# Performance work log

Measured on AMD Instinct MI355X. Metric: run time of the kernel, lower is better.

## Reference

```python
import jax, jax.numpy as jnp
import numpy as np

RADIUS = 1.5
PARTITION_NUM = 5
OUT_CHANNEL = 128
IN_CHANNEL = 64
EPS = 1e-5


def setup_inputs() -> dict:
    key = jax.random.key(0)
    ks = jax.random.split(key, 10)
    B, N, npoint, K = 16, 8192, 2048, 32
    D = 61  # points feature dim; in_channel = D + 3 = 64
    xyz = jax.random.normal(ks[0], (B, N, 3), dtype=jnp.float32)
    points = jax.random.normal(ks[1], (B, N, D), dtype=jnp.float32)
    local_coordinates = jax.random.uniform(ks[2], (B, npoint, K, 3), dtype=jnp.float32)
    neighbor_lists = jax.random.randint(ks[3], (B, npoint, K), 0, N)
    data_idx = jax.random.randint(ks[4], (B, npoint), 0, N)
    parameter_list = jnp.zeros((1,), dtype=jnp.float32)
    # params (torch Linear stored transposed here: [in, out])
    W1 = jax.random.normal(ks[5], (IN_CHANNEL * PARTITION_NUM, OUT_CHANNEL), dtype=jnp.float32) * 0.02
    b1 = jnp.zeros((OUT_CHANNEL,), dtype=jnp.float32)
    g1 = jnp.ones((OUT_CHANNEL,), dtype=jnp.float32)
    be1 = jnp.zeros((OUT_CHANNEL,), dtype=jnp.float32)
    W2 = jax.random.normal(ks[6], (OUT_CHANNEL, OUT_CHANNEL), dtype=jnp.float32) * 0.02
    b2 = jnp.zeros((OUT_CHANNEL,), dtype=jnp.float32)
    g2 = jnp.ones((OUT_CHANNEL,), dtype=jnp.float32)
    be2 = jnp.zeros((OUT_CHANNEL,), dtype=jnp.float32)
    return dict(xyz=xyz, points=points, local_coordinates=local_coordinates,
                neighbor_lists=neighbor_lists, parameter_list=parameter_list,
                data_idx=data_idx, W1=W1, b1=b1, g1=g1, be1=be1,
                W2=W2, b2=b2, g2=g2, be2=be2)


def _forward(xyz, points, local_coordinates, parameter_list,
             W1, b1, g1, be1, W2, b2, g2, be2, neighbor_lists, data_idx):
    B, N, _ = xyz.shape
    _, npoint, K = neighbor_lists.shape
    # new_xyz = index_points(xyz, data_idx)
    new_xyz = jnp.take_along_axis(xyz, data_idx[:, :, None], axis=1)  # [B, npoint, 3]
    # points = cat(points, xyz) -> in_channel features
    pts = jnp.concatenate([points, xyz], axis=2)  # [B, N, C]
    C = pts.shape[-1]
    # gather neighbor feats: [B, npoint, K, C] (permute chain in torch is a net identity)
    idx = neighbor_lists.reshape(B, npoint * K)
    grouped = jnp.take_along_axis(pts, idx[:, :, None], axis=1).reshape(B, npoint, K, C)
    # circle_conv: radial binning + scatter-add over partition bins
    lc = local_coordinates.reshape(B, npoint, K, 3)
    dist = jnp.linalg.norm(lc[..., 0:2], axis=-1)          # [B, npoint, K]
    dist = jnp.minimum(dist / RADIUS, 0.99)                # cut(x, 0.99)
    bins = jnp.floor(dist * PARTITION_NUM).astype(jnp.int32)
    onehot = jax.nn.one_hot(bins, PARTITION_NUM, dtype=grouped.dtype)  # [B, npoint, K, P]
    feature = jnp.einsum('bnkp,bnkc->bnpc', onehot, grouped)           # scatter_add
    feature = feature.reshape(B * npoint, PARTITION_NUM * C)
    # Linear + BatchNorm1d (training-mode batch stats) + ReLU
    x = feature @ W1 + b1                                  # [B*npoint, out]
    mu = x.mean(axis=0)
    var = x.var(axis=0)
    x = jax.nn.relu(g1 * (x - mu) / jnp.sqrt(var + EPS) + be1)
    x = x.reshape(B, npoint, -1)
    # Linear + BatchNorm1d over channels + ReLU
    y = x @ W2 + b2                                        # [B, npoint, out]
    mu2 = y.mean(axis=(0, 1))
    var2 = y.var(axis=(0, 1))
    new_points = jax.nn.relu(g2 * (y - mu2) / jnp.sqrt(var2 + EPS) + be2)
    return new_xyz, new_points


def reference(xyz, points, local_coordinates, neighbor_lists, parameter_list,
              data_idx, W1, b1, g1, be1, W2, b2, g2, be2):
    return _forward(xyz, points, local_coordinates, parameter_list,
                    W1, b1, g1, be1, W2, b2, g2, be2, neighbor_lists, data_idx)
```

## Files before the change

### kernel.cpp

```cpp
#include <hip/hip_runtime.h>
#include <hip/hip_bf16.h>
#include <math.h>

#define B_SZ     16
#define N_PTS    8192
#define NPOINT   2048
#define KNBR     32
#define D_FEAT   61
#define C_IN     64
#define P_BINS   5
#define C_OUT    128
#define M_ROWS   (B_SZ * NPOINT)
#define K1       (C_IN * P_BINS)
#define EPSV     1e-5f
#define NREP     16

typedef __attribute__((ext_vector_type(8))) short bf16x8;
typedef __attribute__((ext_vector_type(4))) float f32x4;

__device__ __forceinline__ unsigned short f2bf_rne(float v) {
    unsigned u = __float_as_uint(v);
    u += 0x7fffu + ((u >> 16) & 1u);
    return (unsigned short)(u >> 16);
}
__device__ __forceinline__ float bf2f(unsigned short v) {
    return __uint_as_float(((unsigned)v) << 16);
}

__device__ __forceinline__ size_t fragB_idx(int n, int c) {
    return ((size_t)((c >> 5) * 8 + (n >> 4)) << 9) +
           ((((c >> 3) & 3) * 16 + (n & 15)) << 3) + (c & 7);
}

__global__ __launch_bounds__(256) void prep_kernel(
    const float* __restrict__ points, const float* __restrict__ xyz,
    const float* __restrict__ W1, const float* __restrict__ W2,
    unsigned short* __restrict__ ptsb, unsigned short* __restrict__ W1f,
    unsigned short* __restrict__ W2f, float* __restrict__ st)
{
    const int blk = blockIdx.x;
    const int tid = threadIdx.x;
    if (blk < 32768) {
        const int xcd  = blk & 7;
        const int slot = blk >> 3;
        const int b    = 2 * xcd + (slot >> 11);
        const int rin  = (slot & 2047) * 4 + (tid >> 6);
        const int row  = b * N_PTS + rin;
        const int c    = tid & 63;
        float v;
        if (c < D_FEAT) v = points[(size_t)row * D_FEAT + c];
        else            v = xyz[(size_t)row * 3 + (c - D_FEAT)];
        ptsb[((size_t)row << 6) | c] = f2bf_rne(v);
    } else {
        const int gid = (blk - 32768) * 256 + tid;
        if (gid < 40960) {
            int c = gid >> 7, n = gid & 127;
            W1f[fragB_idx(n, c)] = f2bf_rne(W1[gid]);
        } else if (gid < 57344) {
            int i = gid - 40960;
            int c = i >> 7, n = i & 127;
            W2f[fragB_idx(n, c)] = f2bf_rne(W2[i]);
        } else {
            st[gid - 57344] = 0.f;
        }
    }
}

__global__ __launch_bounds__(256) void fusedg1_kernel(
    const unsigned short* __restrict__ ptsb, const float* __restrict__ xyz,
    const float* __restrict__ lc, const int* __restrict__ nl,
    const int* __restrict__ didx, const unsigned short* __restrict__ W1f,
    const float* __restrict__ b1, unsigned short* __restrict__ x1f,
    float* __restrict__ st, float* __restrict__ newxyz)
{
    const int g    = blockIdx.x;
    const int xcd  = g & 7;
    const int slot = g >> 3;
    const int b    = 2 * xcd + (slot >> 7);
    const int tile = b * 128 + (slot & 127);
    const int wave = threadIdx.x >> 6;
    const int lane = threadIdx.x & 63;
    const int k    = lane & 31;
    const int lm   = lane & 15, kg = lane >> 4;
    const int kgl  = (lane >> 3) & 3, jl = lane & 7, khalf = lane >> 5;

    __shared__ int s_srt[4][32];
    __shared__ __align__(16) unsigned short sA[10 * 512];

    const unsigned short* __restrict__ tb = ptsb + (((size_t)b * N_PTS) << 6);
    const float* __restrict__ xbase = xyz + (size_t)b * N_PTS * 3;

    for (int p = 0; p < 4; ++p) {
        const int mloc = wave * 4 + p;
        const int bid  = tile * 16 + mloc;
        const size_t nbase = (size_t)bid * KNBR;

        const float x = lc[(nbase + k) * 3 + 0];
        const float y = lc[(nbase + k) * 3 + 1];
        const float dd = fminf(sqrtf(x * x + y * y) * (1.0f / 1.5f), 0.99f);
        int bin = (int)(dd * 5.0f);
        bin = bin > 4 ? 4 : (bin < 0 ? 0 : bin);
        const int n = nl[nbase + k];

        unsigned m0 = (unsigned)__ballot(bin == 0);
        unsigned m1 = (unsigned)__ballot(bin == 1);
        unsigned m2 = (unsigned)__ballot(bin == 2);
        unsigned m3 = (unsigned)__ballot(bin == 3);
        unsigned m4 = (unsigned)__ballot(bin == 4);
        const int c0n = __popc(m0), c1n = __popc(m1);
        const int c2n = __popc(m2), c3n = __popc(m3);
        const int e0 = c0n, e1 = e0 + c1n, e2 = e1 + c2n, e3 = e2 + c3n;

        int start = (bin > 0 ? c0n : 0) + (bin > 1 ? c1n : 0) +
                    (bin > 2 ? c2n : 0) + (bin > 3 ? c3n : 0);
        unsigned mymask = m0;
        mymask = bin == 1 ? m1 : mymask;
        mymask = bin == 2 ? m2 : mymask;
        mymask = bin == 3 ? m3 : mymask;
        mymask = bin == 4 ? m4 : mymask;
        const int pos = start + __popc(mymask & ((1u << k) - 1u));

        if (lane < 32) s_srt[wave][pos] = n;
        if (lane >= 32 && lane < 35) {
            const int di = didx[bid];
            newxyz[(size_t)bid * 3 + (lane - 32)] = xbase[(size_t)di * 3 + (lane - 32)];
        }

        const int srtv = s_srt[wave][k];

        unsigned short vv[32];
        #pragma unroll
        for (int kk = 0; kk < 32; ++kk) {
            const int nr = __builtin_amdgcn_readlane(srtv, kk);
            vv[kk] = tb[((size_t)nr << 6) | lane];
        }

        float a0 = 0.f, a1 = 0.f, a2 = 0.f, a3 = 0.f, a4 = 0.f;
        #pragma unroll
        for (int kk = 0; kk < 32; ++kk) {
            const float v = bf2f(vv[kk]);
            if      (kk < e0) a0 += v;
            else if (kk < e1) a1 += v;
            else if (kk < e2) a2 += v;
            else if (kk < e3) a3 += v;
            else              a4 += v;
        }

        const float vals[5] = {a0, a1, a2, a3, a4};
        #pragma unroll
        for (int bb = 0; bb < 5; ++bb) {
            const int kb = bb * 2 + khalf;
            sA[kb * 512 + (kgl * 16 + mloc) * 8 + jl] = f2bf_rne(vals[bb]);
        }
    }
    __syncthreads();

    f32x4 acc0 = {}, acc1 = {};
    #pragma unroll
    for (int kb = 0; kb < 10; ++kb) {
        bf16x8 a = *(const bf16x8*)&sA[kb * 512 + lane * 8];
        bf16x8 w0 = *(const bf16x8*)(W1f + ((size_t)(kb * 8 + wave * 2) << 9) + lane * 8);
        bf16x8 w1 = *(const bf16x8*)(W1f + ((size_t)(kb * 8 + wave * 2 + 1) << 9) + lane * 8);
        acc0 = __builtin_amdgcn_mfma_f32_16x16x32_bf16(a, w0, acc0, 0, 0, 0);
        acc1 = __builtin_amdgcn_mfma_f32_16x16x32_bf16(a, w1, acc1, 0, 0, 0);
    }

    const int rep = (g & (NREP - 1)) * 128;
    #pragma unroll
    for (int q = 0; q < 2; ++q) {
        const f32x4 A = q ? acc1 : acc0;
        const int col = (wave * 2 + q) * 16 + lm;
        const float bb = b1[col];
        float ls = 0.f, lq = 0.f;
        #pragma unroll
        for (int i = 0; i < 4; ++i) {
            float vv2 = A[i] + bb;
            const size_t idx = (((size_t)(tile * 4 + (col >> 5))) << 9) +
                               ((((col >> 3) & 3) * 16 + kg * 4 + i) << 3) + (col & 7);
            x1f[idx] = f2bf_rne(vv2);
            ls += vv2; lq += vv2 * vv2;
        }
        ls += __shfl_xor(ls, 16); ls += __shfl_xor(ls, 32);
        lq += __shfl_xor(lq, 16); lq += __shfl_xor(lq, 32);
        if (kg == 0) {
            atomicAdd(&st[rep + col], ls);
            atomicAdd(&st[2048 + rep + col], lq);
        }
    }
}

__global__ __launch_bounds__(256) void gemm2_mfma(
    const unsigned short* __restrict__ Xf,
    const float* __restrict__ st_in,
    const float* __restrict__ g1, const float* __restrict__ be1,
    const unsigned short* __restrict__ Wf, const float* __restrict__ bias,
    unsigned short* __restrict__ out, float* __restrict__ st)
{
    __shared__ float sc[128], sh[128];
    const int tid = threadIdx.x;
    if (tid < 128) {
        float s = 0.f, q = 0.f;
        #pragma unroll
        for (int r = 0; r < NREP; ++r) {
            s += st_in[r * 128 + tid];
            q += st_in[2048 + r * 128 + tid];
        }
        float mu  = s * (1.0f / (float)M_ROWS);
        float var = q * (1.0f / (float)M_ROWS) - mu * mu;
        float iv  = 1.0f / sqrtf(var + EPSV);
        float sg  = g1[tid] * iv;
        sc[tid] = sg;
        sh[tid] = be1[tid] - mu * sg;
    }
    __syncthreads();

    const int g    = blockIdx.x;
    const int xcd  = g & 7;
    const int slot = g >> 3;
    const int b    = 2 * xcd + (slot >> 7);
    const int tile = b * 128 + (slot & 127);

    const int wave = tid >> 6, lane = tid & 63;
    const int lm = lane & 15, kg = lane >> 4;

    f32x4 acc0 = {}, acc1 = {};
    #pragma unroll
    for (int kb = 0; kb < 4; ++kb) {
        const int c0 = kb * 32 + kg * 8;
        bf16x8 xr = *(const bf16x8*)(Xf + (((size_t)(tile * 4 + kb)) << 9) + lane * 8);
        bf16x8 a;
        #pragma unroll
        for (int j = 0; j < 8; ++j) {
            float xv = bf2f((unsigned short)xr[j]);
            a[j] = (short)f2bf_rne(fmaxf(0.f, sc[c0 + j] * xv + sh[c0 + j]));
        }
        bf16x8 w0 = *(const bf16x8*)(Wf + ((size_t)(kb * 8 + wave * 2) << 9) + lane * 8);
        bf16x8 w1 = *(const bf16x8*)(Wf + ((size_t)(kb * 8 + wave * 2 + 1) << 9) + lane * 8);
        acc0 = __builtin_amdgcn_mfma_f32_16x16x32_bf16(a, w0, acc0, 0, 0, 0);
        acc1 = __builtin_amdgcn_mfma_f32_16x16x32_bf16(a, w1, acc1, 0, 0, 0);
    }

    const int orow = tile * 16 + kg * 4;
    const int rep = (g & (NREP - 1)) * 128;
    #pragma unroll
    for (int q = 0; q < 2; ++q) {
        const f32x4 A = q ? acc1 : acc0;
        const int col = (wave * 2 + q) * 16 + lm;
        const float bb = bias[col];
        float ls = 0.f, lq = 0.f;
        #pragma unroll
        for (int i = 0; i < 4; ++i) {
            float v = A[i] + bb;
            out[(size_t)(orow + i) * C_OUT + col] = f2bf_rne(v);
            ls += v; lq += v * v;
        }
        ls += __shfl_xor(ls, 16); ls += __shfl_xor(ls, 32);
        lq += __shfl_xor(lq, 16); lq += __shfl_xor(lq, 32);
        if (kg == 0) {
            atomicAdd(&st[4096 + rep + col], ls);
            atomicAdd(&st[6144 + rep + col], lq);
        }
    }
}

__global__ __launch_bounds__(256) void out_kernel(
    const unsigned short* __restrict__ Y, const float* __restrict__ st,
    const float* __restrict__ g2, const float* __restrict__ be2,
    float* __restrict__ out)
{
    __shared__ float sc[128], sh[128];
    const int tid = threadIdx.x;
    if (tid < 128) {
        float s = 0.f, q = 0.f;
        #pragma unroll
        for (int r = 0; r < NREP; ++r) {
            s += st[4096 + r * 128 + tid];
            q += st[6144 + r * 128 + tid];
        }
        float mu  = s * (1.0f / (float)M_ROWS);
        float var = q * (1.0f / (float)M_ROWS) - mu * mu;
        float iv  = 1.0f / sqrtf(var + EPSV);
        float sg  = g2[tid] * iv;
        sc[tid] = sg;
        sh[tid] = be2[tid] - mu * sg;
    }
    __syncthreads();

    const size_t e8 = (size_t)blockIdx.x * 256 + tid;
    bf16x8 v = ((const bf16x8*)Y)[e8];
    const int cb = (int)((e8 * 8) & 127);
    float4 r0, r1;
    r0.x = fmaxf(0.f, sc[cb + 0] * bf2f((unsigned short)v[0]) + sh[cb + 0]);
    r0.y = fmaxf(0.f, sc[cb + 1] * bf2f((unsigned short)v[1]) + sh[cb + 1]);
    r0.z = fmaxf(0.f, sc[cb + 2] * bf2f((unsigned short)v[2]) + sh[cb + 2]);
    r0.w = fmaxf(0.f, sc[cb + 3] * bf2f((unsigned short)v[3]) + sh[cb + 3]);
    r1.x = fmaxf(0.f, sc[cb + 4] * bf2f((unsigned short)v[4]) + sh[cb + 4]);
    r1.y = fmaxf(0.f, sc[cb + 5] * bf2f((unsigned short)v[5]) + sh[cb + 5]);
    r1.z = fmaxf(0.f, sc[cb + 6] * bf2f((unsigned short)v[6]) + sh[cb + 6]);
    r1.w = fmaxf(0.f, sc[cb + 7] * bf2f((unsigned short)v[7]) + sh[cb + 7]);
    ((float4*)out)[e8 * 2]     = r0;
    ((float4*)out)[e8 * 2 + 1] = r1;
}

extern "C" void kernel_launch(void* const* d_in, const int* in_sizes, int n_in,
                              void* d_out, int out_size, void* d_ws, size_t ws_size,
                              hipStream_t stream)
{
    const float* xyz    = (const float*)d_in[0];
    const float* points = (const float*)d_in[1];
    const float* lc     = (const float*)d_in[2];
    const int*   nl     = (const int*)d_in[3];
    const int*   didx   = (const int*)d_in[5];
    const float* W1     = (const float*)d_in[6];
    const float* b1     = (const float*)d_in[7];
    const float* g1     = (const float*)d_in[8];
    const float* be1    = (const float*)d_in[9];
    const float* W2     = (const float*)d_in[10];
    const float* b2     = (const float*)d_in[11];
    const float* g2     = (const float*)d_in[12];
    const float* be2    = (const float*)d_in[13];

    float* out = (float*)d_out;
    char*  ws  = (char*)d_ws;

    unsigned short* ptsb = (unsigned short*)ws;
    unsigned short* x1f  = (unsigned short*)(ws + 16777216);
    unsigned short* yb   = (unsigned short*)(ws + 25165824);
    unsigned short* W1f  = (unsigned short*)(ws + 33554432);
    unsigned short* W2f  = (unsigned short*)(ws + 33636352);
    float*          st   = (float*)(ws + 33669120);

    prep_kernel<<<32768 + 256, 256, 0, stream>>>(points, xyz, W1, W2,
                                                 ptsb, W1f, W2f, st);
    fusedg1_kernel<<<M_ROWS / 16, 256, 0, stream>>>(ptsb, xyz, lc, nl, didx,
                                                    W1f, b1, x1f, st, out);
    gemm2_mfma<<<M_ROWS / 16, 256, 0, stream>>>(x1f, st, g1, be1,
                                                W2f, b2, yb, st);
    out_kernel<<<(M_ROWS * C_OUT) / (256 * 8), 256, 0, stream>>>(
        yb, st, g2, be2, out + (size_t)M_ROWS * 3);
}
```

Measured before the change: 188.1 us.

## Vectorize neighbor gathers via LDS staging and retile gemm2 per-wave with block-reduced stats

Neighbor feature rows are now fetched as 16-byte vector loads, 8 lanes per row, and staged through shared memory. This replaces 32 scalar 2-byte gathers per lane. gemm2 now assigns each wave its own 16-row tile covering all 128 columns, launches 4x fewer blocks, and reduces BN statistics across waves in LDS before issuing atomics. The stat replication factor drops from 16 to 8, which cuts atomic traffic but raises contention per slot, and the extra LDS staging adds shared-memory use and a read-after-write dependency within each wave.

After: 186.6 us. No clear change (-0.8%).

```diff
diff --git a/kernel.cpp b/kernel.cpp
--- a/kernel.cpp
+++ b/kernel.cpp
@@ -13,7 +13,6 @@
 #define M_ROWS   (B_SZ * NPOINT)
 #define K1       (C_IN * P_BINS)
 #define EPSV     1e-5f
-#define NREP     16
 
 typedef __attribute__((ext_vector_type(8))) short bf16x8;
 typedef __attribute__((ext_vector_type(4))) float f32x4;
@@ -60,7 +59,7 @@
             int i = gid - 40960;
             int c = i >> 7, n = i & 127;
             W2f[fragB_idx(n, c)] = f2bf_rne(W2[i]);
-        } else {
+        } else if (gid < 61440) {
             st[gid - 57344] = 0.f;
         }
     }
@@ -85,6 +84,7 @@
     const int kgl  = (lane >> 3) & 3, jl = lane & 7, khalf = lane >> 5;
 
     __shared__ int s_srt[4][32];
+    __shared__ __align__(16) unsigned short s_stage[4][32][64];
     __shared__ __align__(16) unsigned short sA[10 * 512];
 
     const unsigned short* __restrict__ tb = ptsb + (((size_t)b * N_PTS) << 6);
@@ -126,19 +126,18 @@
             newxyz[(size_t)bid * 3 + (lane - 32)] = xbase[(size_t)di * 3 + (lane - 32)];
         }
 
-        const int srtv = s_srt[wave][k];
-
-        unsigned short vv[32];
+        const int r = lane >> 3, j7 = lane & 7;
+        #pragma unroll
+        for (int g4 = 0; g4 < 4; ++g4) {
+            const int nr = s_srt[wave][g4 * 8 + r];
+            bf16x8 row = *(const bf16x8*)(tb + ((size_t)nr << 6) + j7 * 8);
+            *(bf16x8*)&s_stage[wave][g4 * 8 + r][j7 * 8] = row;
+        }
+
+        float a0 = 0.f, a1 = 0.f, a2 = 0.f, a3 = 0.f, a4 = 0.f;
         #pragma unroll
         for (int kk = 0; kk < 32; ++kk) {
-            const int nr = __builtin_amdgcn_readlane(srtv, kk);
-            vv[kk] = tb[((size_t)nr << 6) | lane];
-        }
-
-        float a0 = 0.f, a1 = 0.f, a2 = 0.f, a3 = 0.f, a4 = 0.f;
-        #pragma unroll
-        for (int kk = 0; kk < 32; ++kk) {
-            const float v = bf2f(vv[kk]);
+            const float v = bf2f(s_stage[wave][kk][lane]);
             if      (kk < e0) a0 += v;
             else if (kk < e1) a1 += v;
             else if (kk < e2) a2 += v;
@@ -165,7 +164,7 @@
         acc1 = __builtin_amdgcn_mfma_f32_16x16x32_bf16(a, w1, acc1, 0, 0, 0);
     }
 
-    const int rep = (g & (NREP - 1)) * 128;
+    const int rep = (g & 7) * 128;
     #pragma unroll
     for (int q = 0; q < 2; ++q) {
         const f32x4 A = q ? acc1 : acc0;
@@ -184,7 +183,7 @@
         lq += __shfl_xor(lq, 16); lq += __shfl_xor(lq, 32);
         if (kg == 0) {
             atomicAdd(&st[rep + col], ls);
-            atomicAdd(&st[2048 + rep + col], lq);
+            atomicAdd(&st[1024 + rep + col], lq);
         }
     }
 }
@@ -197,13 +196,14 @@
     unsigned short* __restrict__ out, float* __restrict__ st)
 {
     __shared__ float sc[128], sh[128];
+    __shared__ float s_s[4][128], s_q[4][128];
     const int tid = threadIdx.x;
     if (tid < 128) {
         float s = 0.f, q = 0.f;
         #pragma unroll
-        for (int r = 0; r < NREP; ++r) {
+        for (int r = 0; r < 8; ++r) {
             s += st_in[r * 128 + tid];
-            q += st_in[2048 + r * 128 + tid];
+            q += st_in[1024 + r * 128 + tid];
         }
         float mu  = s * (1.0f / (float)M_ROWS);
         float var = q * (1.0f / (float)M_ROWS) - mu * mu;
@@ -217,13 +217,13 @@
     const int g    = blockIdx.x;
     const int xcd  = g & 7;
     const int slot = g >> 3;
-    const int b    = 2 * xcd + (slot >> 7);
-    const int tile = b * 128 + (slot & 127);
+    const int bb_  = 2 * xcd + (slot >> 5);
+    const int tile = (bb_ * 32 + (slot & 31)) * 4 + (tid >> 6);
 
     const int wave = tid >> 6, lane = tid & 63;
     const int lm = lane & 15, kg = lane >> 4;
 
-    f32x4 acc0 = {}, acc1 = {};
+    f32x4 acc[8] = {};
     #pragma unroll
     for (int kb = 0; kb < 4; ++kb) {
         const int c0 = kb * 32 + kg * 8;
@@ -234,32 +234,36 @@
             float xv = bf2f((unsigned short)xr[j]);
             a[j] = (short)f2bf_rne(fmaxf(0.f, sc[c0 + j] * xv + sh[c0 + j]));
         }
-        bf16x8 w0 = *(const bf16x8*)(Wf + ((size_t)(kb * 8 + wave * 2) << 9) + lane * 8);
-        bf16x8 w1 = *(const bf16x8*)(Wf + ((size_t)(kb * 8 + wave * 2 + 1) << 9) + lane * 8);
-        acc0 = __builtin_amdgcn_mfma_f32_16x16x32_bf16(a, w0, acc0, 0, 0, 0);
-        acc1 = __builtin_amdgcn_mfma_f32_16x16x32_bf16(a, w1, acc1, 0, 0, 0);
+        #pragma unroll
+        for (int nf = 0; nf < 8; ++nf) {
+            bf16x8 bfr = *(const bf16x8*)(Wf + (((size_t)(kb * 8 + nf)) << 9) + lane * 8);
+            acc[nf] = __builtin_amdgcn_mfma_f32_16x16x32_bf16(a, bfr, acc[nf], 0, 0, 0);
+        }
     }
 
     const int orow = tile * 16 + kg * 4;
-    const int rep = (g & (NREP - 1)) * 128;
     #pragma unroll
-    for (int q = 0; q < 2; ++q) {
-        const f32x4 A = q ? acc1 : acc0;
-        const int col = (wave * 2 + q) * 16 + lm;
+    for (int nf = 0; nf < 8; ++nf) {
+        const int col = nf * 16 + lm;
         const float bb = bias[col];
         float ls = 0.f, lq = 0.f;
         #pragma unroll
         for (int i = 0; i < 4; ++i) {
-            float v = A[i] + bb;
+            float v = acc[nf][i] + bb;
             out[(size_t)(orow + i) * C_OUT + col] = f2bf_rne(v);
             ls += v; lq += v * v;
         }
         ls += __shfl_xor(ls, 16); ls += __shfl_xor(ls, 32);
         lq += __shfl_xor(lq, 16); lq += __shfl_xor(lq, 32);
-        if (kg == 0) {
-            atomicAdd(&st[4096 + rep + col], ls);
-            atomicAdd(&st[6144 + rep + col], lq);
-        }
+        if (kg == 0) { s_s[wave][col] = ls; s_q[wave][col] = lq; }
+    }
+    __syncthreads();
+    if (tid < 128) {
+        const int rep = (g & 7) * 128;
+        float ts = s_s[0][tid] + s_s[1][tid] + s_s[2][tid] + s_s[3][tid];
+        float tq = s_q[0][tid] + s_q[1][tid] + s_q[2][tid] + s_q[3][tid];
+        atomicAdd(&st[2048 + rep + tid], ts);
+        atomicAdd(&st[3072 + rep + tid], tq);
     }
 }
 
@@ -273,9 +277,9 @@
     if (tid < 128) {
         float s = 0.f, q = 0.f;
         #pragma unroll
-        for (int r = 0; r < NREP; ++r) {
-            s += st[4096 + r * 128 + tid];
-            q += st[6144 + r * 128 + tid];
+        for (int r = 0; r < 8; ++r) {
+            s += st[2048 + r * 128 + tid];
+            q += st[3072 + r * 128 + tid];
         }
         float mu  = s * (1.0f / (float)M_ROWS);
         float var = q * (1.0f / (float)M_ROWS) - mu * mu;
@@ -334,7 +338,7 @@
                                                  ptsb, W1f, W2f, st);
     fusedg1_kernel<<<M_ROWS / 16, 256, 0, stream>>>(ptsb, xyz, lc, nl, didx,
                                                     W1f, b1, x1f, st, out);
-    gemm2_mfma<<<M_ROWS / 16, 256, 0, stream>>>(x1f, st, g1, be1,
+    gemm2_mfma<<<M_ROWS / 64, 256, 0, stream>>>(x1f, st, g1, be1,
                                                 W2f, b2, yb, st);
     out_kernel<<<(M_ROWS * C_OUT) / (256 * 8), 256, 0, stream>>>(
         yb, st, g2, be2, out + (size_t)M_ROWS * 3);
```
